# Performance work log

Hardware: AMD Instinct MI355X
Metric: run time of the kernel (lower is better)

Reference implementation:

```python
import jax, jax.numpy as jnp
import numpy as np

EMBED_DIM = 128
ATTN_DIM = 64


def setup_inputs() -> dict:
    key = jax.random.key(0)
    kb, kt, kw1, kb1, kw2, kb2 = jax.random.split(key, 6)
    B, S, E = 2048, 200, EMBED_DIM
    behaviors = jax.random.normal(kb, (B, S, E), dtype=jnp.float32)
    target = jax.random.normal(kt, (B, E), dtype=jnp.float32)
    # Linear params (torch nn.Linear: y = x @ W.T + b); store as [in, out] for einsum
    lim1 = 1.0 / np.sqrt(4 * E)
    W1 = jax.random.uniform(kw1, (4 * E, ATTN_DIM), jnp.float32, -lim1, lim1)
    b1 = jax.random.uniform(kb1, (ATTN_DIM,), jnp.float32, -lim1, lim1)
    lim2 = 1.0 / np.sqrt(ATTN_DIM)
    W2 = jax.random.uniform(kw2, (ATTN_DIM, 1), jnp.float32, -lim2, lim2)
    b2 = jax.random.uniform(kb2, (1,), jnp.float32, -lim2, lim2)
    return {"behaviors": behaviors, "target": target, "W1": W1, "b1": b1, "W2": W2, "b2": b2}


def reference(behaviors, target, W1, b1, W2, b2):
    # behaviors: [B,S,E], target: [B,E] -> broadcast to [B,S,E]
    t = target[:, None, :]  # broadcast instead of repeat
    feat = jnp.concatenate([behaviors,
                            jnp.broadcast_to(t, behaviors.shape),
                            behaviors * t,
                            behaviors - t], axis=-1)  # [B,S,4E]
    h = jax.nn.relu(jnp.einsum('bsf,fa->bsa', feat, W1) + b1)  # [B,S,A]
    w = jax.nn.sigmoid(jnp.einsum('bsa,ao->bso', h, W2) + b2)  # [B,S,1]
    return jnp.sum(w * behaviors, axis=1)  # [B,E]
```

## Files before the change

### kernel.cpp

```cpp
#include <hip/hip_runtime.h>

typedef __attribute__((ext_vector_type(8))) short bf16x8;
typedef __attribute__((ext_vector_type(4))) float f32x4;

__device__ __forceinline__ short f2bf(float f) {
    union { float f; unsigned u; } v; v.f = f;
    unsigned r = (v.u + 0x7FFFu + ((v.u >> 16) & 1u)) >> 16;
    return (short)r;
}

__device__ __forceinline__ float sigmoidf(float x) {
    return 1.0f / (1.0f + __expf(-x));
}

constexpr int S = 200, E = 128, A = 64;
constexpr int BSTR = 132;
constexpr int WSTR = 136;

__global__ __launch_bounds__(256, 3) void attn_fused(
    const float* __restrict__ behaviors,
    const float* __restrict__ target,
    const float* __restrict__ W1,
    const float* __restrict__ b1,
    const float* __restrict__ W2,
    const float* __restrict__ b2,
    float* __restrict__ out)
{
    __shared__ float b_lds[64 * BSTR];
    __shared__ short wb_lds[A * WSTR];
    __shared__ float t_lds[E];
    __shared__ float bias_lds[A];
    __shared__ float w2_lds[A];
    __shared__ float w_lds[64];

    const int tid  = threadIdx.x;
    const int bat  = blockIdx.x;
    const int lane = tid & 63;
    const int wave = tid >> 6;
    const int l15  = lane & 15;
    const int quad = lane >> 4;

    if (tid < E) t_lds[tid] = target[(size_t)bat * E + tid];
    __syncthreads();

    for (int i = tid; i < E * A; i += 256) {
        const int e = i >> 6, a = i & 63;
        const float wa = W1[e * A + a];
        const float wd = W1[(384 + e) * A + a];
        const float wc = W1[(256 + e) * A + a];
        wb_lds[a * WSTR + e] = f2bf(wa + wd + t_lds[e] * wc);
    }
    if (tid < A) {
        float acc = b1[tid];
        for (int e = 0; e < E; ++e)
            acc += t_lds[e] * (W1[(128 + e) * A + tid] - W1[(384 + e) * A + tid]);
        bias_lds[tid] = acc;
        w2_lds[tid] = W2[tid];
    }
    __syncthreads();

    bf16x8 bfrag[4][4];
    #pragma unroll
    for (int kt = 0; kt < 4; ++kt)
        #pragma unroll
        for (int nt = 0; nt < 4; ++nt)
            bfrag[kt][nt] = *(const bf16x8*)&wb_lds[(nt*16 + l15) * WSTR + kt*32 + quad*8];

    float bias_l[4], w2_l[4];
    #pragma unroll
    for (int nt = 0; nt < 4; ++nt) {
        bias_l[nt] = bias_lds[nt*16 + l15];
        w2_l[nt]   = w2_lds[nt*16 + l15];
    }
    const float b2v = b2[0];

    const float* bptr = behaviors + (size_t)bat * S * E;
    const int c4  = tid & 31;
    const int grp = tid >> 5;
    f32x4 oacc = {0.f, 0.f, 0.f, 0.f};

    for (int r = 0; r < 4; ++r) {
        #pragma unroll
        for (int j = 0; j < 8; ++j) {
            const int i   = tid + j * 256;
            const int row = i >> 5;
            const int col = i & 31;
            const int srow = r * 64 + row;
            f32x4 v = {0.f, 0.f, 0.f, 0.f};
            if (srow < S) v = *(const f32x4*)(bptr + srow * E + col * 4);
            *(f32x4*)&b_lds[row * BSTR + col * 4] = v;
        }
        __syncthreads();

        f32x4 acc[4];
        #pragma unroll
        for (int nt = 0; nt < 4; ++nt) acc[nt] = f32x4{0.f, 0.f, 0.f, 0.f};

        const float* arow = &b_lds[(wave*16 + l15) * BSTR + quad*8];
        #pragma unroll
        for (int kt = 0; kt < 4; ++kt) {
            f32x4 a0 = *(const f32x4*)(arow + kt*32);
            f32x4 a1 = *(const f32x4*)(arow + kt*32 + 4);
            bf16x8 af;
            af[0] = f2bf(a0[0]); af[1] = f2bf(a0[1]);
            af[2] = f2bf(a0[2]); af[3] = f2bf(a0[3]);
            af[4] = f2bf(a1[0]); af[5] = f2bf(a1[1]);
            af[6] = f2bf(a1[2]); af[7] = f2bf(a1[3]);
            #pragma unroll
            for (int nt = 0; nt < 4; ++nt)
                acc[nt] = __builtin_amdgcn_mfma_f32_16x16x32_bf16(af, bfrag[kt][nt], acc[nt], 0, 0, 0);
        }

        float wgt[4];
        #pragma unroll
        for (int reg = 0; reg < 4; ++reg) {
            float p = 0.f;
            #pragma unroll
            for (int nt = 0; nt < 4; ++nt) {
                float h = acc[nt][reg] + bias_l[nt];
                p += fmaxf(h, 0.f) * w2_l[nt];
            }
            #pragma unroll
            for (int off = 1; off < 16; off <<= 1)
                p += __shfl_xor(p, off, 64);
            wgt[reg] = sigmoidf(p + b2v);
        }
        if (l15 == 0) {
            #pragma unroll
            for (int reg = 0; reg < 4; ++reg)
                w_lds[wave*16 + quad*4 + reg] = wgt[reg];
        }
        __syncthreads();

        f32x4 w0 = *(const f32x4*)&w_lds[grp*8];
        f32x4 w1v = *(const f32x4*)&w_lds[grp*8 + 4];
        #pragma unroll
        for (int s = 0; s < 8; ++s) {
            const float w = (s < 4) ? w0[s] : w1v[s - 4];
            f32x4 bv = *(const f32x4*)&b_lds[(grp*8 + s) * BSTR + c4*4];
            oacc[0] += w * bv[0]; oacc[1] += w * bv[1];
            oacc[2] += w * bv[2]; oacc[3] += w * bv[3];
        }
        __syncthreads();
    }

    float* red = b_lds;
    *(f32x4*)&red[grp * 128 + c4*4] = oacc;
    __syncthreads();
    if (tid < 128) {
        float s = 0.f;
        #pragma unroll
        for (int g = 0; g < 8; ++g) s += red[g * 128 + tid];
        out[(size_t)bat * E + tid] = s;
    }
}

extern "C" void kernel_launch(void* const* d_in, const int* in_sizes, int n_in,
                              void* d_out, int out_size, void* d_ws, size_t ws_size,
                              hipStream_t stream) {
    const float* behaviors = (const float*)d_in[0];
    const float* target    = (const float*)d_in[1];
    const float* W1        = (const float*)d_in[2];
    const float* b1        = (const float*)d_in[3];
    const float* W2        = (const float*)d_in[4];
    const float* b2        = (const float*)d_in[5];
    float* out = (float*)d_out;

    hipLaunchKernelGGL(attn_fused, dim3(2048), dim3(256), 0, stream,
                       behaviors, target, W1, b1, W2, b2, out);
}
```

Baseline: 361.1 us.

## Keep behavior rows in registers per wave and drop LDS staging of behaviors

Each wave now processes 16-row strips of behaviors loaded straight from global memory into registers, reusing those registers for both the MFMA score computation and the weighted sum. This removes the LDS staging buffer and the per-tile block barriers. Weights are pre-swizzled into fragment order in LDS and read per MFMA instead of held in registers. The bias reduction is split across all threads, and occupancy is raised to 4 blocks. The cost is extra shuffle reductions and more per-thread accumulator registers.

Result: no change. 355.1 us (-1.7%).

```diff
diff --git a/kernel.cpp b/kernel.cpp
--- a/kernel.cpp
+++ b/kernel.cpp
@@ -14,10 +14,9 @@
 }
 
 constexpr int S = 200, E = 128, A = 64;
-constexpr int BSTR = 132;
-constexpr int WSTR = 136;
-
-__global__ __launch_bounds__(256, 3) void attn_fused(
+constexpr int NSTRIP = 13;
+
+__global__ __launch_bounds__(256, 4) void attn_fused(
     const float* __restrict__ behaviors,
     const float* __restrict__ target,
     const float* __restrict__ W1,
@@ -26,12 +25,12 @@
     const float* __restrict__ b2,
     float* __restrict__ out)
 {
-    __shared__ float b_lds[64 * BSTR];
-    __shared__ short wb_lds[A * WSTR];
+    __shared__ short wb_f[16 * 512];
+    __shared__ short wbtmp[E * A];
+    __shared__ float red[4 * 128];
     __shared__ float t_lds[E];
     __shared__ float bias_lds[A];
     __shared__ float w2_lds[A];
-    __shared__ float w_lds[64];
 
     const int tid  = threadIdx.x;
     const int bat  = blockIdx.x;
@@ -45,70 +44,81 @@
 
     for (int i = tid; i < E * A; i += 256) {
         const int e = i >> 6, a = i & 63;
-        const float wa = W1[e * A + a];
-        const float wd = W1[(384 + e) * A + a];
-        const float wc = W1[(256 + e) * A + a];
-        wb_lds[a * WSTR + e] = f2bf(wa + wd + t_lds[e] * wc);
-    }
+        wbtmp[i] = f2bf(W1[e * A + a] + W1[(384 + e) * A + a]
+                        + t_lds[e] * W1[(256 + e) * A + a]);
+    }
+    {
+        const int a = tid & 63, seg = tid >> 6;
+        float acc = 0.f;
+        for (int e = seg * 32; e < seg * 32 + 32; ++e)
+            acc += t_lds[e] * (W1[(128 + e) * A + a] - W1[(384 + e) * A + a]);
+        red[seg * 64 + a] = acc;
+    }
+    __syncthreads();
     if (tid < A) {
-        float acc = b1[tid];
-        for (int e = 0; e < E; ++e)
-            acc += t_lds[e] * (W1[(128 + e) * A + tid] - W1[(384 + e) * A + tid]);
-        bias_lds[tid] = acc;
+        bias_lds[tid] = b1[tid] + red[tid] + red[64 + tid] + red[128 + tid] + red[192 + tid];
         w2_lds[tid] = W2[tid];
     }
-    __syncthreads();
-
-    bf16x8 bfrag[4][4];
-    #pragma unroll
-    for (int kt = 0; kt < 4; ++kt)
-        #pragma unroll
-        for (int nt = 0; nt < 4; ++nt)
-            bfrag[kt][nt] = *(const bf16x8*)&wb_lds[(nt*16 + l15) * WSTR + kt*32 + quad*8];
+    for (int i = tid; i < E * A; i += 256) {
+        const int j = i & 7, ln = (i >> 3) & 63, frag = i >> 9;
+        const int kt = frag >> 2, nt = frag & 3;
+        const int n = nt * 16 + (ln & 15);
+        const int k = kt * 32 + (ln >> 4) * 8 + j;
+        wb_f[i] = wbtmp[k * A + n];
+    }
+    __syncthreads();
 
     float bias_l[4], w2_l[4];
     #pragma unroll
     for (int nt = 0; nt < 4; ++nt) {
-        bias_l[nt] = bias_lds[nt*16 + l15];
-        w2_l[nt]   = w2_lds[nt*16 + l15];
+        bias_l[nt] = bias_lds[nt * 16 + l15];
+        w2_l[nt]   = w2_lds[nt * 16 + l15];
     }
     const float b2v = b2[0];
-
     const float* bptr = behaviors + (size_t)bat * S * E;
-    const int c4  = tid & 31;
-    const int grp = tid >> 5;
-    f32x4 oacc = {0.f, 0.f, 0.f, 0.f};
-
-    for (int r = 0; r < 4; ++r) {
-        #pragma unroll
-        for (int j = 0; j < 8; ++j) {
-            const int i   = tid + j * 256;
-            const int row = i >> 5;
-            const int col = i & 31;
-            const int srow = r * 64 + row;
-            f32x4 v = {0.f, 0.f, 0.f, 0.f};
-            if (srow < S) v = *(const f32x4*)(bptr + srow * E + col * 4);
-            *(f32x4*)&b_lds[row * BSTR + col * 4] = v;
-        }
-        __syncthreads();
+
+    f32x4 oacc[4][2];
+    #pragma unroll
+    for (int kt = 0; kt < 4; ++kt) {
+        oacc[kt][0] = f32x4{0.f, 0.f, 0.f, 0.f};
+        oacc[kt][1] = f32x4{0.f, 0.f, 0.f, 0.f};
+    }
+
+    for (int st = wave; st < NSTRIP; st += 4) {
+        const int row = st * 16 + l15;
+        const bool valid = (row < S);
+        const float* rp = bptr + (size_t)row * E + quad * 8;
+
+        f32x4 av[4][2];
+        #pragma unroll
+        for (int kt = 0; kt < 4; ++kt) {
+            av[kt][0] = f32x4{0.f, 0.f, 0.f, 0.f};
+            av[kt][1] = f32x4{0.f, 0.f, 0.f, 0.f};
+        }
+        if (valid) {
+            #pragma unroll
+            for (int kt = 0; kt < 4; ++kt) {
+                av[kt][0] = *(const f32x4*)(rp + kt * 32);
+                av[kt][1] = *(const f32x4*)(rp + kt * 32 + 4);
+            }
+        }
 
         f32x4 acc[4];
         #pragma unroll
         for (int nt = 0; nt < 4; ++nt) acc[nt] = f32x4{0.f, 0.f, 0.f, 0.f};
 
-        const float* arow = &b_lds[(wave*16 + l15) * BSTR + quad*8];
-        #pragma unroll
-        for (int kt = 0; kt < 4; ++kt) {
-            f32x4 a0 = *(const f32x4*)(arow + kt*32);
-            f32x4 a1 = *(const f32x4*)(arow + kt*32 + 4);
+        #pragma unroll
+        for (int kt = 0; kt < 4; ++kt) {
             bf16x8 af;
-            af[0] = f2bf(a0[0]); af[1] = f2bf(a0[1]);
-            af[2] = f2bf(a0[2]); af[3] = f2bf(a0[3]);
-            af[4] = f2bf(a1[0]); af[5] = f2bf(a1[1]);
-            af[6] = f2bf(a1[2]); af[7] = f2bf(a1[3]);
-            #pragma unroll
-            for (int nt = 0; nt < 4; ++nt)
-                acc[nt] = __builtin_amdgcn_mfma_f32_16x16x32_bf16(af, bfrag[kt][nt], acc[nt], 0, 0, 0);
+            af[0] = f2bf(av[kt][0][0]); af[1] = f2bf(av[kt][0][1]);
+            af[2] = f2bf(av[kt][0][2]); af[3] = f2bf(av[kt][0][3]);
+            af[4] = f2bf(av[kt][1][0]); af[5] = f2bf(av[kt][1][1]);
+            af[6] = f2bf(av[kt][1][2]); af[7] = f2bf(av[kt][1][3]);
+            #pragma unroll
+            for (int nt = 0; nt < 4; ++nt) {
+                bf16x8 bf = *(const bf16x8*)&wb_f[(kt * 4 + nt) * 512 + lane * 8];
+                acc[nt] = __builtin_amdgcn_mfma_f32_16x16x32_bf16(af, bf, acc[nt], 0, 0, 0);
+            }
         }
 
         float wgt[4];
@@ -117,41 +127,61 @@
             float p = 0.f;
             #pragma unroll
             for (int nt = 0; nt < 4; ++nt) {
-                float h = acc[nt][reg] + bias_l[nt];
+                const float h = acc[nt][reg] + bias_l[nt];
                 p += fmaxf(h, 0.f) * w2_l[nt];
             }
-            #pragma unroll
-            for (int off = 1; off < 16; off <<= 1)
-                p += __shfl_xor(p, off, 64);
+            p += __shfl_xor(p, 1, 64);
+            p += __shfl_xor(p, 2, 64);
+            p += __shfl_xor(p, 4, 64);
+            p += __shfl_xor(p, 8, 64);
             wgt[reg] = sigmoidf(p + b2v);
         }
-        if (l15 == 0) {
-            #pragma unroll
-            for (int reg = 0; reg < 4; ++reg)
-                w_lds[wave*16 + quad*4 + reg] = wgt[reg];
-        }
-        __syncthreads();
-
-        f32x4 w0 = *(const f32x4*)&w_lds[grp*8];
-        f32x4 w1v = *(const f32x4*)&w_lds[grp*8 + 4];
-        #pragma unroll
-        for (int s = 0; s < 8; ++s) {
-            const float w = (s < 4) ? w0[s] : w1v[s - 4];
-            f32x4 bv = *(const f32x4*)&b_lds[(grp*8 + s) * BSTR + c4*4];
-            oacc[0] += w * bv[0]; oacc[1] += w * bv[1];
-            oacc[2] += w * bv[2]; oacc[3] += w * bv[3];
-        }
-        __syncthreads();
-    }
-
-    float* red = b_lds;
-    *(f32x4*)&red[grp * 128 + c4*4] = oacc;
-    __syncthreads();
-    if (tid < 128) {
-        float s = 0.f;
-        #pragma unroll
-        for (int g = 0; g < 8; ++g) s += red[g * 128 + tid];
-        out[(size_t)bat * E + tid] = s;
+
+        const int srcl = (l15 >> 2) << 4;
+        const float t0 = __shfl(wgt[0], srcl, 64);
+        const float t1 = __shfl(wgt[1], srcl, 64);
+        const float t2 = __shfl(wgt[2], srcl, 64);
+        const float t3 = __shfl(wgt[3], srcl, 64);
+        const float wl = (l15 & 2) ? ((l15 & 1) ? t3 : t2)
+                                   : ((l15 & 1) ? t1 : t0);
+
+        #pragma unroll
+        for (int kt = 0; kt < 4; ++kt) {
+            #pragma unroll
+            for (int h = 0; h < 2; ++h) {
+                oacc[kt][h][0] += wl * av[kt][h][0];
+                oacc[kt][h][1] += wl * av[kt][h][1];
+                oacc[kt][h][2] += wl * av[kt][h][2];
+                oacc[kt][h][3] += wl * av[kt][h][3];
+            }
+        }
+    }
+
+    #pragma unroll
+    for (int kt = 0; kt < 4; ++kt)
+        #pragma unroll
+        for (int h = 0; h < 2; ++h)
+            #pragma unroll
+            for (int c = 0; c < 4; ++c) {
+                float v = oacc[kt][h][c];
+                v += __shfl_xor(v, 1, 64);
+                v += __shfl_xor(v, 2, 64);
+                v += __shfl_xor(v, 4, 64);
+                v += __shfl_xor(v, 8, 64);
+                oacc[kt][h][c] = v;
+            }
+
+    if (l15 == 0) {
+        #pragma unroll
+        for (int kt = 0; kt < 4; ++kt) {
+            *(f32x4*)&red[wave * 128 + kt * 32 + quad * 8]     = oacc[kt][0];
+            *(f32x4*)&red[wave * 128 + kt * 32 + quad * 8 + 4] = oacc[kt][1];
+        }
+    }
+    __syncthreads();
+    if (tid < E) {
+        out[(size_t)bat * E + tid] =
+            red[tid] + red[128 + tid] + red[256 + tid] + red[384 + tid];
     }
 }
 
```
